# Performance work log

Measured on AMD Instinct MI355X. Metric: run time of the kernel, lower is better.

The kernel has to match this reference:

```python
import jax, jax.numpy as jnp
import numpy as np

HEADS = 8
CH = 256
DH = CH // HEADS  # 32
NB = 128          # nb_features
EPS = 1e-4


def setup_inputs() -> dict:
    key = jax.random.key(0)
    ks = jax.random.split(key, 8)
    b, c, h, w = 4, CH, 96, 96
    s = 1.0 / np.sqrt(CH)  # typical linear init scale
    x = jax.random.normal(ks[0], (b, c, h, w), dtype=jnp.float32)
    wq = jax.random.normal(ks[1], (CH, CH), dtype=jnp.float32) * s
    wk = jax.random.normal(ks[2], (CH, CH), dtype=jnp.float32) * s
    wv = jax.random.normal(ks[3], (CH, CH), dtype=jnp.float32) * s
    wo = jax.random.normal(ks[4], (CH, CH), dtype=jnp.float32) * s
    bo = jnp.zeros((CH,), dtype=jnp.float32)
    # FAVOR+ gaussian orthogonal random projection (nb_features, dim_head)
    pm = np.random.default_rng(0)
    blocks = []
    for _ in range(NB // DH):
        qmat, _ = np.linalg.qr(pm.standard_normal((DH, DH)))
        blocks.append(qmat.T)
    proj = np.concatenate(blocks, axis=0)
    # scale rows to chi-distributed norms (scaling=0 default in performer_pytorch)
    norms = np.linalg.norm(pm.standard_normal((NB, DH)), axis=1, keepdims=True)
    proj_mat = jnp.asarray(proj * norms, dtype=jnp.float32)
    wp = jax.random.normal(ks[5], (CH, CH, 1, 1), dtype=jnp.float32) * s
    bp = jnp.zeros((CH,), dtype=jnp.float32)
    return {"x": x, "wq": wq, "wk": wk, "wv": wv, "wo": wo, "bo": bo,
            "proj_mat": proj_mat, "wp": wp, "bp": bp}


def softmax_kernel(data, proj, is_query):
    # data: (b, h, n, d); proj: (m, d). Performer FAVOR+ positive softmax features.
    data_normalizer = data.shape[-1] ** -0.25
    ratio = proj.shape[0] ** -0.5
    data_dash = jnp.einsum('bhnd,md->bhnm', data * data_normalizer, proj)
    diag = (jnp.sum(data * data, axis=-1) * 0.5 * (data_normalizer ** 2))[..., None]
    if is_query:
        m = jnp.max(data_dash, axis=-1, keepdims=True)
    else:
        m = jnp.max(data_dash, axis=(-1, -2), keepdims=True)
    return ratio * (jnp.exp(data_dash - diag - m) + EPS)


def reference(x, wq, wk, wv, wo, bo, proj_mat, wp, bp):
    b, c, h, w = x.shape
    n = h * w
    xf = x.reshape(b, c, n).transpose(0, 2, 1)  # (b, n, c)

    def split_heads(t):
        return t.reshape(b, n, HEADS, DH).transpose(0, 2, 1, 3)  # (b, h, n, d)

    q = split_heads(xf @ wq.T)
    k = split_heads(xf @ wk.T)
    v = split_heads(xf @ wv.T)

    qp = softmax_kernel(q, proj_mat, True)   # (b, h, n, m)
    kp = softmax_kernel(k, proj_mat, False)  # (b, h, n, m)

    # non-causal linear attention
    k_sum = jnp.sum(kp, axis=-2)                                   # (b, h, m)
    d_inv = 1.0 / jnp.einsum('bhnm,bhm->bhn', qp, k_sum)           # (b, h, n)
    ctx = jnp.einsum('bhnm,bhnd->bhmd', kp, v)                     # (b, h, m, d)
    out = jnp.einsum('bhnm,bhmd->bhnd', qp, ctx) * d_inv[..., None]

    out = out.transpose(0, 2, 1, 3).reshape(b, n, c)  # merge heads
    out = out @ wo.T + bo                              # to_out (attn_out_bias=True)
    out = out.transpose(0, 2, 1).reshape(b, c, h, w)
    # 1x1 conv projection
    out = jnp.einsum('bchw,oc->bohw', out, wp[:, :, 0, 0]) + bp[None, :, None, None]
    return out
```

## Files before the change

### kernel.cpp

```cpp
#include <hip/hip_runtime.h>

#define NTOT 9216
#define NORMC 0.42044820762685725f
#define RATIO 0.08838834764831845f
#define FEPS 1e-4f

typedef _Float16 h8 __attribute__((ext_vector_type(8)));
typedef _Float16 h4 __attribute__((ext_vector_type(4)));
typedef float f4 __attribute__((ext_vector_type(4)));

__device__ __forceinline__ void gld16(const _Float16* g, _Float16* l) {
  __builtin_amdgcn_global_load_lds((const __attribute__((address_space(1))) void*)g,
                                   (__attribute__((address_space(3))) void*)l, 16, 0, 0);
}

__global__ __launch_bounds__(256) void prep(
    const float* __restrict__ x, const float* __restrict__ wq,
    const float* __restrict__ wk, const float* __restrict__ wv,
    const float* __restrict__ proj, const float* __restrict__ wo,
    const float* __restrict__ bo, const float* __restrict__ wp,
    const float* __restrict__ bp, _Float16* __restrict__ xT,
    _Float16* __restrict__ Wall, _Float16* __restrict__ projh,
    _Float16* __restrict__ Wc, float* __restrict__ bc) {
  __shared__ float T_s[64][65];
  int r = blockIdx.x, t = threadIdx.x;
  if (r < 2304) {
    int nx = r % 144, rem = r / 144;
    int cy = rem & 3, b = rem >> 2;
    int n0 = nx * 64, c0 = cy * 64;
    for (int i = 0; i < 4; ++i) {
      int f = t + i * 256;
      int cc = f >> 4, n4 = f & 15;
      float4 a = *(const float4*)(x + ((size_t)(b * 256 + c0 + cc)) * NTOT + n0 + n4 * 4);
      T_s[cc][n4 * 4 + 0] = a.x;
      T_s[cc][n4 * 4 + 1] = a.y;
      T_s[cc][n4 * 4 + 2] = a.z;
      T_s[cc][n4 * 4 + 3] = a.w;
    }
    __syncthreads();
    for (int i = 0; i < 2; ++i) {
      int f = t + i * 256;
      int nn = f >> 3, c8 = f & 7;
      h8 hv;
      for (int j = 0; j < 8; ++j) hv[j] = (_Float16)T_s[c8 * 8 + j][nn];
      *(h8*)(xT + ((size_t)(b * NTOT + n0 + nn)) * 256 + c0 + c8 * 8) = hv;
    }
    return;
  }
  int r2 = r - 2304;
  if (r2 < 768) {
    const float* src = (r2 < 256) ? wq + (size_t)r2 * 256
                     : (r2 < 512) ? wk + (size_t)(r2 - 256) * 256
                                  : wv + (size_t)(r2 - 512) * 256;
    Wall[(size_t)r2 * 256 + t] = (_Float16)src[t];
  } else if (r2 < 784) {
    int idx = (r2 - 768) * 256 + t;
    projh[idx] = (_Float16)proj[idx];
  } else {
    int o = r2 - 784;
    float acc = 0.f;
    for (int c = 0; c < 256; ++c) acc += wp[o * 256 + c] * wo[c * 256 + t];
    Wc[o * 256 + t] = (_Float16)acc;
    if (t == 0) {
      float ab = bp[o];
      for (int c = 0; c < 256; ++c) ab += wp[o * 256 + c] * bo[c];
      bc[o] = ab;
    }
  }
}

__global__ __launch_bounds__(256) void qkv_mfma(
    const _Float16* __restrict__ xT, const _Float16* __restrict__ Wall,
    const _Float16* __restrict__ projh, _Float16* __restrict__ q,
    _Float16* __restrict__ k, _Float16* __restrict__ vT,
    float* __restrict__ kmaxp) {
  __shared__ __align__(16) _Float16 pool[16384];
  int bx = blockIdx.x, co0 = blockIdx.y * 128, sel = blockIdx.z;
  int b = bx / 72, ntile = bx % 72;
  int n0 = bx * 128;
  const _Float16* Wb = Wall + (size_t)sel * 65536;
  int t = threadIdx.x, wave = t >> 6, lane = t & 63;
  int lm = lane & 15, lg = lane >> 4;
  int wm = (wave & 1) * 64, wn = (wave >> 1) * 64;
  int srow = wave * 32 + (lane >> 2);
  int scol = ((lane & 3) ^ ((lane >> 3) & 3)) * 8;
  const _Float16* gA = Wb + (size_t)(co0 + srow) * 256 + scol;
  const _Float16* gB = xT + (size_t)(n0 + srow) * 256 + scol;
  int so = wave * 1024;
  int pg = (lg ^ ((lm >> 1) & 3)) * 8;
  f4 acc[4][4] = {};
  gld16(gA, pool + so);
  gld16(gA + 16 * 256, pool + so + 512);
  gld16(gB, pool + 8192 + so);
  gld16(gB + 16 * 256, pool + 8192 + so + 512);
#pragma unroll 1
  for (int kt = 0; kt < 7; ++kt) {
    int cur = (kt & 1) << 12;
    int nxt = cur ^ 4096;
    int c0 = (kt + 1) * 32;
    gld16(gA + c0, pool + nxt + so);
    gld16(gA + c0 + 16 * 256, pool + nxt + so + 512);
    gld16(gB + c0, pool + 8192 + nxt + so);
    gld16(gB + c0 + 16 * 256, pool + 8192 + nxt + so + 512);
    asm volatile("s_waitcnt vmcnt(4)" ::: "memory");
    __builtin_amdgcn_s_barrier();
    __builtin_amdgcn_sched_barrier(0);
    h8 a[4], bf[4];
#pragma unroll
    for (int mi = 0; mi < 4; ++mi)
      a[mi] = *(const h8*)&pool[cur + (wm + mi * 16 + lm) * 32 + pg];
#pragma unroll
    for (int ni = 0; ni < 4; ++ni)
      bf[ni] = *(const h8*)&pool[8192 + cur + (wn + ni * 16 + lm) * 32 + pg];
    if (sel < 2) {
#pragma unroll
      for (int mi = 0; mi < 4; ++mi)
#pragma unroll
        for (int ni = 0; ni < 4; ++ni)
          acc[mi][ni] = __builtin_amdgcn_mfma_f32_16x16x32_f16(a[mi], bf[ni], acc[mi][ni], 0, 0, 0);
    } else {
#pragma unroll
      for (int mi = 0; mi < 4; ++mi)
#pragma unroll
        for (int ni = 0; ni < 4; ++ni)
          acc[mi][ni] = __builtin_amdgcn_mfma_f32_16x16x32_f16(bf[ni], a[mi], acc[mi][ni], 0, 0, 0);
    }
    __builtin_amdgcn_s_barrier();
  }
  {
    asm volatile("s_waitcnt vmcnt(0)" ::: "memory");
    __builtin_amdgcn_s_barrier();
    __builtin_amdgcn_sched_barrier(0);
    h8 a[4], bf[4];
#pragma unroll
    for (int mi = 0; mi < 4; ++mi)
      a[mi] = *(const h8*)&pool[4096 + (wm + mi * 16 + lm) * 32 + pg];
#pragma unroll
    for (int ni = 0; ni < 4; ++ni)
      bf[ni] = *(const h8*)&pool[8192 + 4096 + (wn + ni * 16 + lm) * 32 + pg];
    if (sel < 2) {
#pragma unroll
      for (int mi = 0; mi < 4; ++mi)
#pragma unroll
        for (int ni = 0; ni < 4; ++ni)
          acc[mi][ni] = __builtin_amdgcn_mfma_f32_16x16x32_f16(a[mi], bf[ni], acc[mi][ni], 0, 0, 0);
    } else {
#pragma unroll
      for (int mi = 0; mi < 4; ++mi)
#pragma unroll
        for (int ni = 0; ni < 4; ++ni)
          acc[mi][ni] = __builtin_amdgcn_mfma_f32_16x16x32_f16(bf[ni], a[mi], acc[mi][ni], 0, 0, 0);
    }
  }
  if (sel < 2) {
    _Float16* Out = (sel == 0) ? q : k;
#pragma unroll
    for (int mi = 0; mi < 4; ++mi)
#pragma unroll
      for (int ni = 0; ni < 4; ++ni) {
        h4 hv;
#pragma unroll
        for (int r = 0; r < 4; ++r) hv[r] = (_Float16)acc[mi][ni][r];
        *(h4*)(Out + (size_t)(n0 + wn + ni * 16 + lm) * 256 + co0 + wm + mi * 16 + lg * 4) = hv;
      }
    if (sel == 1) {
      _Float16* ktile = pool;
      h8 pr[8];
#pragma unroll
      for (int mt = 0; mt < 8; ++mt)
        pr[mt] = *(const h8*)&projh[(mt * 16 + lm) * 32 + lg * 8];
      float vmax = -1e30f;
      for (int half = 0; half < 2; ++half) {
        __syncthreads();
        if ((wave >> 1) == half) {
#pragma unroll
          for (int mi = 0; mi < 4; ++mi)
#pragma unroll
            for (int ni = 0; ni < 4; ++ni) {
              h4 hv;
#pragma unroll
              for (int r = 0; r < 4; ++r) hv[r] = (_Float16)acc[mi][ni][r];
              *(h4*)&ktile[(ni * 16 + lm) * 132 + wm + mi * 16 + lg * 4] = hv;
            }
        }
        __syncthreads();
#pragma unroll
        for (int nt2 = 0; nt2 < 4; ++nt2) {
          h8 a = *(const h8*)&ktile[(nt2 * 16 + lm) * 132 + wave * 32 + lg * 8];
#pragma unroll
          for (int mt = 0; mt < 8; ++mt) {
            f4 z = {0.f, 0.f, 0.f, 0.f};
            f4 d = __builtin_amdgcn_mfma_f32_16x16x32_f16(a, pr[mt], z, 0, 0, 0);
            vmax = fmaxf(vmax, fmaxf(fmaxf(d[0], d[1]), fmaxf(d[2], d[3])));
          }
        }
      }
      for (int i = 1; i < 64; i <<= 1) vmax = fmaxf(vmax, __shfl_xor(vmax, i, 64));
      if (lane == 0) {
        int h = (co0 >> 5) + wave;
        kmaxp[(size_t)(b * 8 + h) * 72 + ntile] = NORMC * vmax;
      }
    }
  } else {
#pragma unroll
    for (int mi = 0; mi < 4; ++mi)
#pragma unroll
      for (int ni = 0; ni < 4; ++ni) {
        h4 hv;
#pragma unroll
        for (int r = 0; r < 4; ++r) hv[r] = (_Float16)acc[mi][ni][r];
        *(h4*)(vT + ((size_t)(b * 256 + co0 + wm + mi * 16 + lm)) * NTOT +
               ntile * 128 + wn + ni * 16 + lg * 4) = hv;
      }
  }
}

__global__ __launch_bounds__(256) void ctx_mfma(
    const _Float16* __restrict__ k, const _Float16* __restrict__ vT,
    const _Float16* __restrict__ projh, const float* __restrict__ kmaxp,
    float* __restrict__ part) {
  __shared__ __align__(16) _Float16 k_s[128 * 32];
  __shared__ __align__(16) _Float16 vT_s[32 * 136];
  __shared__ __align__(16) _Float16 kpT[128 * 136];
  __shared__ float diag_s[128];
  __shared__ float kmax_sh;
  int bh = blockIdx.y, b = bh >> 3, h = bh & 7;
  int nbase = blockIdx.x * 384;
  int t = threadIdx.x, wave = t >> 6, lane = t & 63, lm = lane & 15, lg = lane >> 4;
  h8 pr[8];
#pragma unroll
  for (int mt = 0; mt < 8; ++mt) pr[mt] = *(const h8*)&projh[(mt * 16 + lm) * 32 + lg * 8];
  int scol = ((lane & 3) ^ ((lane >> 3) & 3)) * 8;
  const _Float16* gK =
      k + ((size_t)(b * NTOT + nbase + wave * 32 + (lane >> 2))) * 256 + h * 32 + scol;
  const _Float16* gV = vT + ((size_t)(b * 256 + h * 32 + (t >> 3))) * NTOT + nbase;
  _Float16* lK = k_s + wave * 1024;
  int vd = t >> 3, vg = t & 7;
  gld16(gK, lK);
  gld16(gK + 16 * 256, lK + 512);
  h8 vr0 = *(const h8*)(gV + vg * 8);
  h8 vr1 = *(const h8*)(gV + 64 + vg * 8);
  {
    float* kred = (float*)kpT;
    if (t < 72) kred[t] = kmaxp[(size_t)bh * 72 + t];
    __syncthreads();
    if (t == 0) {
      float mx = -1e30f;
      for (int i = 0; i < 72; ++i) mx = fmaxf(mx, kred[i]);
      kmax_sh = mx;
    }
    __syncthreads();
  }
  float kmax = kmax_sh;
  int pg = (lg ^ ((lm >> 1) & 3)) * 8;
  f4 cacc[2][2] = {};
  float ks[8] = {};
#pragma unroll 1
  for (int ch = 0; ch < 3; ++ch) {
    *(h8*)&vT_s[vd * 136 + vg * 8] = vr0;
    *(h8*)&vT_s[vd * 136 + 64 + vg * 8] = vr1;
    asm volatile("s_waitcnt vmcnt(0) lgkmcnt(0)" ::: "memory");
    __builtin_amdgcn_s_barrier();
    __builtin_amdgcn_sched_barrier(0);
    if (t < 128) {
      float s = 0.f;
#pragma unroll
      for (int c = 0; c < 4; ++c) {
        h8 kv = *(const h8*)&k_s[t * 32 + c * 8];
#pragma unroll
        for (int j = 0; j < 8; ++j) s += (float)kv[j] * (float)kv[j];
      }
      diag_s[t] = s * (0.5f * NORMC * NORMC);
    }
    f4 dsh[2][8];
#pragma unroll
    for (int nt = 0; nt < 2; ++nt) {
      h8 a = *(const h8*)&k_s[(wave * 32 + nt * 16 + lm) * 32 + pg];
#pragma unroll
      for (int mt = 0; mt < 8; ++mt) {
        f4 z = {0.f, 0.f, 0.f, 0.f};
        dsh[nt][mt] = __builtin_amdgcn_mfma_f32_16x16x32_f16(a, pr[mt], z, 0, 0, 0);
      }
    }
    asm volatile("s_waitcnt lgkmcnt(0)" ::: "memory");
    __builtin_amdgcn_s_barrier();
    __builtin_amdgcn_sched_barrier(0);
    if (ch < 2) {
      gld16(gK + (size_t)((ch + 1) * 128) * 256, lK);
      gld16(gK + (size_t)((ch + 1) * 128) * 256 + 16 * 256, lK + 512);
      vr0 = *(const h8*)(gV + (ch + 1) * 128 + vg * 8);
      vr1 = *(const h8*)(gV + (ch + 1) * 128 + 64 + vg * 8);
    }
#pragma unroll
    for (int nt = 0; nt < 2; ++nt)
#pragma unroll
      for (int mt = 0; mt < 8; ++mt) {
        h4 hv;
        float lsum = 0.f;
#pragma unroll
        for (int r = 0; r < 4; ++r) {
          int nl = wave * 32 + nt * 16 + lg * 4 + r;
          float val = RATIO * (__expf(NORMC * dsh[nt][mt][r] - diag_s[nl] - kmax) + FEPS);
          hv[r] = (_Float16)val;
          lsum += val;
        }
        ks[mt] += lsum;
        *(h4*)&kpT[(mt * 16 + lm) * 136 + wave * 32 + nt * 16 + lg * 4] = hv;
      }
    asm volatile("s_waitcnt lgkmcnt(0)" ::: "memory");
    __builtin_amdgcn_s_barrier();
    __builtin_amdgcn_sched_barrier(0);
#pragma unroll
    for (int k2 = 0; k2 < 4; ++k2) {
      h8 a2[2], b2[2];
#pragma unroll
      for (int mt2 = 0; mt2 < 2; ++mt2)
        a2[mt2] = *(const h8*)&kpT[(wave * 32 + mt2 * 16 + lm) * 136 + k2 * 32 + lg * 8];
#pragma unroll
      for (int dt = 0; dt < 2; ++dt)
        b2[dt] = *(const h8*)&vT_s[(dt * 16 + lm) * 136 + k2 * 32 + lg * 8];
#pragma unroll
      for (int mt2 = 0; mt2 < 2; ++mt2)
#pragma unroll
        for (int dt = 0; dt < 2; ++dt)
          cacc[mt2][dt] =
              __builtin_amdgcn_mfma_f32_16x16x32_f16(a2[mt2], b2[dt], cacc[mt2][dt], 0, 0, 0);
    }
    __builtin_amdgcn_s_barrier();
  }
  float* pp = part + (size_t)(blockIdx.y * 24 + blockIdx.x) * 4224;
#pragma unroll
  for (int mt2 = 0; mt2 < 2; ++mt2)
#pragma unroll
    for (int dt = 0; dt < 2; ++dt)
      *(f4*)(pp + (dt * 16 + lm) * 128 + wave * 32 + mt2 * 16 + lg * 4) = cacc[mt2][dt];
  float* redk = (float*)kpT;
#pragma unroll
  for (int mt = 0; mt < 8; ++mt) {
    float s = ks[mt];
    s += __shfl_xor(s, 16, 64);
    s += __shfl_xor(s, 32, 64);
    if (lg == 0) redk[wave * 128 + mt * 16 + lm] = s;
  }
  __syncthreads();
  if (t < 128)
    pp[32 * 128 + t] = redk[t] + redk[128 + t] + redk[256 + t] + redk[384 + t];
}

__global__ __launch_bounds__(256) void reduce_ctx(
    const float* __restrict__ part, _Float16* __restrict__ ctxT_g,
    float* __restrict__ ksum_g) {
  int bh = blockIdx.x >> 2, qtr = blockIdx.x & 3;
  int t = threadIdx.x;
  const float* pb = part + (size_t)bh * 24 * 4224;
  for (int it = 0; it < 5; ++it) {
    int lc = it * 256 + t;
    if (lc < 1056) {
      int cell = qtr * 1056 + lc;
      float s = 0.f;
      for (int p = 0; p < 24; ++p) s += pb[(size_t)p * 4224 + cell];
      int d = cell >> 7, m = cell & 127;
      if (d < 32) ctxT_g[(size_t)bh * 4096 + d * 128 + m] = (_Float16)s;
      else ksum_g[(size_t)bh * 128 + m] = s;
    }
  }
}

__global__ __launch_bounds__(256) void attn_mfma(
    const _Float16* __restrict__ q, const _Float16* __restrict__ projh,
    const _Float16* __restrict__ ctxT_g, const float* __restrict__ ksum_g,
    _Float16* __restrict__ attn) {
  __shared__ __align__(16) _Float16 q_sh[128 * 32];
  __shared__ __align__(16) _Float16 qp_s[128 * 136];
  __shared__ float ksum_s[128];
  int n0 = blockIdx.x * 128;
  int bh = blockIdx.y, b = bh >> 3, h = bh & 7;
  int t = threadIdx.x, wave = t >> 6, lane = t & 63, lm = lane & 15, lg = lane >> 4;
  h8 pr[8];
#pragma unroll
  for (int mt = 0; mt < 8; ++mt) pr[mt] = *(const h8*)&projh[(mt * 16 + lm) * 32 + lg * 8];
  int scol = ((lane & 3) ^ ((lane >> 3) & 3)) * 8;
  const _Float16* gQ =
      q + ((size_t)(b * NTOT + n0 + wave * 32 + (lane >> 2))) * 256 + h * 32 + scol;
  gld16(gQ, q_sh + wave * 1024);
  gld16(gQ + 16 * 256, q_sh + wave * 1024 + 512);
  h8 ac[2][4];
#pragma unroll
  for (int dt = 0; dt < 2; ++dt)
#pragma unroll
    for (int k2 = 0; k2 < 4; ++k2)
      ac[dt][k2] = *(const h8*)&ctxT_g[(size_t)bh * 4096 + (dt * 16 + lm) * 128 + k2 * 32 + lg * 8];
  if (t < 128) ksum_s[t] = ksum_g[(size_t)bh * 128 + t];
  __syncthreads();
  int pg = (lg ^ ((lm >> 1) & 3)) * 8;
  float diag_r[2];
#pragma unroll
  for (int nt = 0; nt < 2; ++nt) {
    int n = wave * 32 + nt * 16 + lm;
    float s = 0.f;
#pragma unroll
    for (int c = 0; c < 4; ++c) {
      h8 qv = *(const h8*)&q_sh[n * 32 + c * 8];
#pragma unroll
      for (int j = 0; j < 8; ++j) s += (float)qv[j] * (float)qv[j];
    }
    diag_r[nt] = s * (0.5f * NORMC * NORMC);
  }
  f4 dsh[2][8];
#pragma unroll
  for (int nt = 0; nt < 2; ++nt) {
    h8 qf = *(const h8*)&q_sh[(wave * 32 + nt * 16 + lm) * 32 + pg];
#pragma unroll
    for (int mt = 0; mt < 8; ++mt) {
      f4 z = {0.f, 0.f, 0.f, 0.f};
      dsh[nt][mt] = __builtin_amdgcn_mfma_f32_16x16x32_f16(pr[mt], qf, z, 0, 0, 0);
    }
  }
  float den_r[2];
#pragma unroll
  for (int nt = 0; nt < 2; ++nt) {
    float mx = -1e30f;
#pragma unroll
    for (int mt = 0; mt < 8; ++mt)
#pragma unroll
      for (int r = 0; r < 4; ++r) mx = fmaxf(mx, dsh[nt][mt][r]);
    mx = fmaxf(mx, __shfl_xor(mx, 16, 64));
    mx = fmaxf(mx, __shfl_xor(mx, 32, 64));
    float den = 0.f;
#pragma unroll
    for (int mt = 0; mt < 8; ++mt) {
      h4 hv;
#pragma unroll
      for (int r = 0; r < 4; ++r) {
        float val = RATIO * (__expf(NORMC * (dsh[nt][mt][r] - mx) - diag_r[nt]) + FEPS);
        hv[r] = (_Float16)val;
        den += val * ksum_s[mt * 16 + lg * 4 + r];
      }
      *(h4*)&qp_s[(wave * 32 + nt * 16 + lm) * 136 + mt * 16 + lg * 4] = hv;
    }
    den += __shfl_xor(den, 16, 64);
    den += __shfl_xor(den, 32, 64);
    den_r[nt] = 1.f / den;
  }
  __syncthreads();
  f4 oacc[2][2] = {};
#pragma unroll
  for (int k2 = 0; k2 < 4; ++k2) {
    h8 bq[2];
#pragma unroll
    for (int nt = 0; nt < 2; ++nt)
      bq[nt] = *(const h8*)&qp_s[(wave * 32 + nt * 16 + lm) * 136 + k2 * 32 + lg * 8];
#pragma unroll
    for (int dt = 0; dt < 2; ++dt)
#pragma unroll
      for (int nt = 0; nt < 2; ++nt)
        oacc[dt][nt] = __builtin_amdgcn_mfma_f32_16x16x32_f16(ac[dt][k2], bq[nt], oacc[dt][nt], 0, 0, 0);
  }
#pragma unroll
  for (int dt = 0; dt < 2; ++dt)
#pragma unroll
    for (int nt = 0; nt < 2; ++nt) {
      int n = wave * 32 + nt * 16 + lm;
      h4 hv;
#pragma unroll
      for (int r = 0; r < 4; ++r) hv[r] = (_Float16)(oacc[dt][nt][r] * den_r[nt]);
      *(h4*)(attn + ((size_t)(b * NTOT + n0 + n)) * 256 + h * 32 + dt * 16 + lg * 4) = hv;
    }
}

__global__ __launch_bounds__(256) void out_mfma(
    const _Float16* __restrict__ Wc, const _Float16* __restrict__ attn,
    const float* __restrict__ bc, float* __restrict__ out) {
  __shared__ __align__(16) _Float16 pool[16384];
  int bx = blockIdx.x;
  int o0 = blockIdx.y * 128;
  int b = bx / 72, nb0 = (bx % 72) * 128;
  int t = threadIdx.x, wave = t >> 6, lane = t & 63;
  int lm = lane & 15, lg = lane >> 4;
  int wm = (wave & 1) * 64, wn = (wave >> 1) * 64;
  int srow = wave * 32 + (lane >> 2);
  int scol = ((lane & 3) ^ ((lane >> 3) & 3)) * 8;
  const _Float16* gA = Wc + (size_t)(o0 + srow) * 256 + scol;
  const _Float16* gB = attn + (size_t)(b * NTOT + nb0 + srow) * 256 + scol;
  int so = wave * 1024;
  int pg = (lg ^ ((lm >> 1) & 3)) * 8;
  f4 acc[4][4] = {};
  gld16(gA, pool + so);
  gld16(gA + 16 * 256, pool + so + 512);
  gld16(gB, pool + 8192 + so);
  gld16(gB + 16 * 256, pool + 8192 + so + 512);
#pragma unroll 1
  for (int kt = 0; kt < 7; ++kt) {
    int cur = (kt & 1) << 12;
    int nxt = cur ^ 4096;
    int c0 = (kt + 1) * 32;
    gld16(gA + c0, pool + nxt + so);
    gld16(gA + c0 + 16 * 256, pool + nxt + so + 512);
    gld16(gB + c0, pool + 8192 + nxt + so);
    gld16(gB + c0 + 16 * 256, pool + 8192 + nxt + so + 512);
    asm volatile("s_waitcnt vmcnt(4)" ::: "memory");
    __builtin_amdgcn_s_barrier();
    __builtin_amdgcn_sched_barrier(0);
    h8 a[4], bf[4];
#pragma unroll
    for (int mi = 0; mi < 4; ++mi)
      a[mi] = *(const h8*)&pool[cur + (wm + mi * 16 + lm) * 32 + pg];
#pragma unroll
    for (int ni = 0; ni < 4; ++ni)
      bf[ni] = *(const h8*)&pool[8192 + cur + (wn + ni * 16 + lm) * 32 + pg];
#pragma unroll
    for (int mi = 0; mi < 4; ++mi)
#pragma unroll
      for (int ni = 0; ni < 4; ++ni)
        acc[mi][ni] = __builtin_amdgcn_mfma_f32_16x16x32_f16(bf[ni], a[mi], acc[mi][ni], 0, 0, 0);
    __builtin_amdgcn_s_barrier();
  }
  {
    asm volatile("s_waitcnt vmcnt(0)" ::: "memory");
    __builtin_amdgcn_s_barrier();
    __builtin_amdgcn_sched_barrier(0);
    h8 a[4], bf[4];
#pragma unroll
    for (int mi = 0; mi < 4; ++mi)
      a[mi] = *(const h8*)&pool[4096 + (wm + mi * 16 + lm) * 32 + pg];
#pragma unroll
    for (int ni = 0; ni < 4; ++ni)
      bf[ni] = *(const h8*)&pool[8192 + 4096 + (wn + ni * 16 + lm) * 32 + pg];
#pragma unroll
    for (int mi = 0; mi < 4; ++mi)
#pragma unroll
      for (int ni = 0; ni < 4; ++ni)
        acc[mi][ni] = __builtin_amdgcn_mfma_f32_16x16x32_f16(bf[ni], a[mi], acc[mi][ni], 0, 0, 0);
  }
#pragma unroll
  for (int mi = 0; mi < 4; ++mi) {
    int o = o0 + wm + mi * 16 + lm;
    float bias = bc[o];
#pragma unroll
    for (int ni = 0; ni < 4; ++ni) {
      f4 ov = acc[mi][ni];
      float4 st = make_float4(ov[0] + bias, ov[1] + bias, ov[2] + bias, ov[3] + bias);
      *(float4*)(out + ((size_t)(b * 256 + o)) * NTOT + nb0 + wn + ni * 16 + lg * 4) = st;
    }
  }
}

extern "C" void kernel_launch(void* const* d_in, const int* in_sizes, int n_in,
                              void* d_out, int out_size, void* d_ws, size_t ws_size,
                              hipStream_t stream) {
  const float* x = (const float*)d_in[0];
  const float* wq = (const float*)d_in[1];
  const float* wk = (const float*)d_in[2];
  const float* wv = (const float*)d_in[3];
  const float* wo = (const float*)d_in[4];
  const float* bo = (const float*)d_in[5];
  const float* proj = (const float*)d_in[6];
  const float* wp = (const float*)d_in[7];
  const float* bp = (const float*)d_in[8];
  float* out = (float*)d_out;
  float* ws = (float*)d_ws;

  float* part = ws;
  float* kmaxp = part + 3244032;
  float* ksum_g = kmaxp + 2304;
  float* bc = ksum_g + 4096;
  _Float16* hb = (_Float16*)(bc + 256);
  const size_t THALF = (size_t)4 * NTOT * 256;
  _Float16* q_h = hb;
  _Float16* k_h = q_h + THALF;
  _Float16* xT = k_h + THALF;
  _Float16* vTg = xT + THALF;
  _Float16* Wall = vTg + THALF;
  _Float16* Wc = Wall + 768 * 256;
  _Float16* projh = Wc + 65536;
  _Float16* ctxT_g = projh + 4096;

  prep<<<3344, 256, 0, stream>>>(x, wq, wk, wv, proj, wo, bo, wp, bp,
                                 xT, Wall, projh, Wc, bc);
  qkv_mfma<<<dim3(288, 2, 3), 256, 0, stream>>>(xT, Wall, projh, q_h, k_h, vTg, kmaxp);
  ctx_mfma<<<dim3(24, 32), 256, 0, stream>>>(k_h, vTg, projh, kmaxp, part);
  reduce_ctx<<<128, 256, 0, stream>>>(part, ctxT_g, ksum_g);
  attn_mfma<<<dim3(72, 32), 256, 0, stream>>>(q_h, projh, ctxT_g, ksum_g, xT);
  out_mfma<<<dim3(288, 2), 256, 0, stream>>>(Wc, xT, bc, out);
}
```

Measured before the change: 217.1 us.

## Fuse Q, K, V projections into one block sharing the activation tile

The QKV GEMM kernel now computes all three projections in a single block, loading each activation tile once into shared memory and reusing it against the Wq, Wk and Wv tiles. The grid drops its third dimension. This removes the repeated global loads of xT across three separate blocks and folds the tail iteration into the main loop. In exchange, each block holds three accumulator sets (48 f4 registers) and double-buffers 64KB of LDS, which can lower occupancy and raise register pressure. The out GEMM loop gets the same tail folding.

```diff
diff --git a/kernel.cpp b/kernel.cpp
--- a/kernel.cpp
+++ b/kernel.cpp
@@ -74,144 +74,125 @@
     const _Float16* __restrict__ projh, _Float16* __restrict__ q,
     _Float16* __restrict__ k, _Float16* __restrict__ vT,
     float* __restrict__ kmaxp) {
-  __shared__ __align__(16) _Float16 pool[16384];
-  int bx = blockIdx.x, co0 = blockIdx.y * 128, sel = blockIdx.z;
+  __shared__ __align__(16) _Float16 pool[32768];
+  int bx = blockIdx.x, co0 = blockIdx.y * 128;
   int b = bx / 72, ntile = bx % 72;
   int n0 = bx * 128;
-  const _Float16* Wb = Wall + (size_t)sel * 65536;
   int t = threadIdx.x, wave = t >> 6, lane = t & 63;
   int lm = lane & 15, lg = lane >> 4;
   int wm = (wave & 1) * 64, wn = (wave >> 1) * 64;
   int srow = wave * 32 + (lane >> 2);
   int scol = ((lane & 3) ^ ((lane >> 3) & 3)) * 8;
-  const _Float16* gA = Wb + (size_t)(co0 + srow) * 256 + scol;
   const _Float16* gB = xT + (size_t)(n0 + srow) * 256 + scol;
+  const _Float16* gWq = Wall + (size_t)(co0 + srow) * 256 + scol;
+  const _Float16* gWk = gWq + 65536;
+  const _Float16* gWv = gWq + 131072;
   int so = wave * 1024;
   int pg = (lg ^ ((lm >> 1) & 3)) * 8;
-  f4 acc[4][4] = {};
-  gld16(gA, pool + so);
-  gld16(gA + 16 * 256, pool + so + 512);
-  gld16(gB, pool + 8192 + so);
-  gld16(gB + 16 * 256, pool + 8192 + so + 512);
+  f4 acc_q[4][4] = {}, acc_k[4][4] = {}, acc_v[4][4] = {};
+  gld16(gB, pool + so);
+  gld16(gB + 16 * 256, pool + so + 512);
+  gld16(gWq, pool + 4096 + so);
+  gld16(gWq + 16 * 256, pool + 4096 + so + 512);
+  gld16(gWk, pool + 8192 + so);
+  gld16(gWk + 16 * 256, pool + 8192 + so + 512);
+  gld16(gWv, pool + 12288 + so);
+  gld16(gWv + 16 * 256, pool + 12288 + so + 512);
 #pragma unroll 1
-  for (int kt = 0; kt < 7; ++kt) {
-    int cur = (kt & 1) << 12;
-    int nxt = cur ^ 4096;
-    int c0 = (kt + 1) * 32;
-    gld16(gA + c0, pool + nxt + so);
-    gld16(gA + c0 + 16 * 256, pool + nxt + so + 512);
-    gld16(gB + c0, pool + 8192 + nxt + so);
-    gld16(gB + c0 + 16 * 256, pool + 8192 + nxt + so + 512);
-    asm volatile("s_waitcnt vmcnt(4)" ::: "memory");
+  for (int kt = 0; kt < 8; ++kt) {
+    int cur = (kt & 1) << 14;
+    int nxt = cur ^ 16384;
+    if (kt < 7) {
+      int c0 = (kt + 1) * 32;
+      gld16(gB + c0, pool + nxt + so);
+      gld16(gB + c0 + 16 * 256, pool + nxt + so + 512);
+      gld16(gWq + c0, pool + nxt + 4096 + so);
+      gld16(gWq + c0 + 16 * 256, pool + nxt + 4096 + so + 512);
+      gld16(gWk + c0, pool + nxt + 8192 + so);
+      gld16(gWk + c0 + 16 * 256, pool + nxt + 8192 + so + 512);
+      gld16(gWv + c0, pool + nxt + 12288 + so);
+      gld16(gWv + c0 + 16 * 256, pool + nxt + 12288 + so + 512);
+      asm volatile("s_waitcnt vmcnt(8)" ::: "memory");
+    } else {
+      asm volatile("s_waitcnt vmcnt(0)" ::: "memory");
+    }
     __builtin_amdgcn_s_barrier();
     __builtin_amdgcn_sched_barrier(0);
-    h8 a[4], bf[4];
+    h8 bf[4], aq[4], ak[4], av[4];
+#pragma unroll
+    for (int ni = 0; ni < 4; ++ni)
+      bf[ni] = *(const h8*)&pool[cur + (wn + ni * 16 + lm) * 32 + pg];
+#pragma unroll
+    for (int mi = 0; mi < 4; ++mi) {
+      int ro = (wm + mi * 16 + lm) * 32 + pg;
+      aq[mi] = *(const h8*)&pool[cur + 4096 + ro];
+      ak[mi] = *(const h8*)&pool[cur + 8192 + ro];
+      av[mi] = *(const h8*)&pool[cur + 12288 + ro];
+    }
 #pragma unroll
     for (int mi = 0; mi < 4; ++mi)
-      a[mi] = *(const h8*)&pool[cur + (wm + mi * 16 + lm) * 32 + pg];
-#pragma unroll
-    for (int ni = 0; ni < 4; ++ni)
-      bf[ni] = *(const h8*)&pool[8192 + cur + (wn + ni * 16 + lm) * 32 + pg];
-    if (sel < 2) {
-#pragma unroll
-      for (int mi = 0; mi < 4; ++mi)
-#pragma unroll
-        for (int ni = 0; ni < 4; ++ni)
-          acc[mi][ni] = __builtin_amdgcn_mfma_f32_16x16x32_f16(a[mi], bf[ni], acc[mi][ni], 0, 0, 0);
-    } else {
-#pragma unroll
-      for (int mi = 0; mi < 4; ++mi)
-#pragma unroll
-        for (int ni = 0; ni < 4; ++ni)
-          acc[mi][ni] = __builtin_amdgcn_mfma_f32_16x16x32_f16(bf[ni], a[mi], acc[mi][ni], 0, 0, 0);
-    }
-    __builtin_amdgcn_s_barrier();
-  }
+#pragma unroll
+      for (int ni = 0; ni < 4; ++ni) {
+        acc_q[mi][ni] = __builtin_amdgcn_mfma_f32_16x16x32_f16(aq[mi], bf[ni], acc_q[mi][ni], 0, 0, 0);
+        acc_k[mi][ni] = __builtin_amdgcn_mfma_f32_16x16x32_f16(ak[mi], bf[ni], acc_k[mi][ni], 0, 0, 0);
+        acc_v[mi][ni] = __builtin_amdgcn_mfma_f32_16x16x32_f16(bf[ni], av[mi], acc_v[mi][ni], 0, 0, 0);
+      }
+    __builtin_amdgcn_s_barrier();
+  }
+#pragma unroll
+  for (int mi = 0; mi < 4; ++mi)
+#pragma unroll
+    for (int ni = 0; ni < 4; ++ni) {
+      h4 hq, hk, hv;
+#pragma unroll
+      for (int r = 0; r < 4; ++r) {
+        hq[r] = (_Float16)acc_q[mi][ni][r];
+        hk[r] = (_Float16)acc_k[mi][ni][r];
+        hv[r] = (_Float16)acc_v[mi][ni][r];
+      }
+      size_t nidx = (size_t)(n0 + wn + ni * 16 + lm) * 256 + co0 + wm + mi * 16 + lg * 4;
+      *(h4*)(q + nidx) = hq;
+      *(h4*)(k + nidx) = hk;
+      *(h4*)(vT + ((size_t)(b * 256 + co0 + wm + mi * 16 + lm)) * NTOT +
+             ntile * 128 + wn + ni * 16 + lg * 4) = hv;
+    }
   {
-    asm volatile("s_waitcnt vmcnt(0)" ::: "memory");
-    __builtin_amdgcn_s_barrier();
-    __builtin_amdgcn_sched_barrier(0);
-    h8 a[4], bf[4];
-#pragma unroll
-    for (int mi = 0; mi < 4; ++mi)
-      a[mi] = *(const h8*)&pool[4096 + (wm + mi * 16 + lm) * 32 + pg];
-#pragma unroll
-    for (int ni = 0; ni < 4; ++ni)
-      bf[ni] = *(const h8*)&pool[8192 + 4096 + (wn + ni * 16 + lm) * 32 + pg];
-    if (sel < 2) {
-#pragma unroll
-      for (int mi = 0; mi < 4; ++mi)
-#pragma unroll
-        for (int ni = 0; ni < 4; ++ni)
-          acc[mi][ni] = __builtin_amdgcn_mfma_f32_16x16x32_f16(a[mi], bf[ni], acc[mi][ni], 0, 0, 0);
-    } else {
-#pragma unroll
-      for (int mi = 0; mi < 4; ++mi)
-#pragma unroll
-        for (int ni = 0; ni < 4; ++ni)
-          acc[mi][ni] = __builtin_amdgcn_mfma_f32_16x16x32_f16(bf[ni], a[mi], acc[mi][ni], 0, 0, 0);
-    }
-  }
-  if (sel < 2) {
-    _Float16* Out = (sel == 0) ? q : k;
-#pragma unroll
-    for (int mi = 0; mi < 4; ++mi)
-#pragma unroll
-      for (int ni = 0; ni < 4; ++ni) {
-        h4 hv;
-#pragma unroll
-        for (int r = 0; r < 4; ++r) hv[r] = (_Float16)acc[mi][ni][r];
-        *(h4*)(Out + (size_t)(n0 + wn + ni * 16 + lm) * 256 + co0 + wm + mi * 16 + lg * 4) = hv;
-      }
-    if (sel == 1) {
-      _Float16* ktile = pool;
-      h8 pr[8];
-#pragma unroll
-      for (int mt = 0; mt < 8; ++mt)
-        pr[mt] = *(const h8*)&projh[(mt * 16 + lm) * 32 + lg * 8];
-      float vmax = -1e30f;
-      for (int half = 0; half < 2; ++half) {
-        __syncthreads();
-        if ((wave >> 1) == half) {
-#pragma unroll
-          for (int mi = 0; mi < 4; ++mi)
-#pragma unroll
-            for (int ni = 0; ni < 4; ++ni) {
-              h4 hv;
-#pragma unroll
-              for (int r = 0; r < 4; ++r) hv[r] = (_Float16)acc[mi][ni][r];
-              *(h4*)&ktile[(ni * 16 + lm) * 132 + wm + mi * 16 + lg * 4] = hv;
-            }
+    _Float16* ktile = pool;
+    h8 pr[8];
+#pragma unroll
+    for (int mt = 0; mt < 8; ++mt)
+      pr[mt] = *(const h8*)&projh[(mt * 16 + lm) * 32 + lg * 8];
+    float vmax = -1e30f;
+    for (int half = 0; half < 2; ++half) {
+      __syncthreads();
+      if ((wave >> 1) == half) {
+#pragma unroll
+        for (int mi = 0; mi < 4; ++mi)
+#pragma unroll
+          for (int ni = 0; ni < 4; ++ni) {
+            h4 hv;
+#pragma unroll
+            for (int r = 0; r < 4; ++r) hv[r] = (_Float16)acc_k[mi][ni][r];
+            *(h4*)&ktile[(ni * 16 + lm) * 132 + wm + mi * 16 + lg * 4] = hv;
+          }
+      }
+      __syncthreads();
+#pragma unroll
+      for (int nt2 = 0; nt2 < 4; ++nt2) {
+        h8 a = *(const h8*)&ktile[(nt2 * 16 + lm) * 132 + wave * 32 + lg * 8];
+#pragma unroll
+        for (int mt = 0; mt < 8; ++mt) {
+          f4 z = {0.f, 0.f, 0.f, 0.f};
+          f4 d = __builtin_amdgcn_mfma_f32_16x16x32_f16(a, pr[mt], z, 0, 0, 0);
+          vmax = fmaxf(vmax, fmaxf(fmaxf(d[0], d[1]), fmaxf(d[2], d[3])));
         }
-        __syncthreads();
-#pragma unroll
-        for (int nt2 = 0; nt2 < 4; ++nt2) {
-          h8 a = *(const h8*)&ktile[(nt2 * 16 + lm) * 132 + wave * 32 + lg * 8];
-#pragma unroll
-          for (int mt = 0; mt < 8; ++mt) {
-            f4 z = {0.f, 0.f, 0.f, 0.f};
-            f4 d = __builtin_amdgcn_mfma_f32_16x16x32_f16(a, pr[mt], z, 0, 0, 0);
-            vmax = fmaxf(vmax, fmaxf(fmaxf(d[0], d[1]), fmaxf(d[2], d[3])));
-          }
-        }
-      }
-      for (int i = 1; i < 64; i <<= 1) vmax = fmaxf(vmax, __shfl_xor(vmax, i, 64));
-      if (lane == 0) {
-        int h = (co0 >> 5) + wave;
-        kmaxp[(size_t)(b * 8 + h) * 72 + ntile] = NORMC * vmax;
-      }
-    }
-  } else {
-#pragma unroll
-    for (int mi = 0; mi < 4; ++mi)
-#pragma unroll
-      for (int ni = 0; ni < 4; ++ni) {
-        h4 hv;
-#pragma unroll
-        for (int r = 0; r < 4; ++r) hv[r] = (_Float16)acc[mi][ni][r];
-        *(h4*)(vT + ((size_t)(b * 256 + co0 + wm + mi * 16 + lm)) * NTOT +
-               ntile * 128 + wn + ni * 16 + lg * 4) = hv;
-      }
+      }
+    }
+    for (int i = 1; i < 64; i <<= 1) vmax = fmaxf(vmax, __shfl_xor(vmax, i, 64));
+    if (lane == 0) {
+      int h = (co0 >> 5) + wave;
+      kmaxp[(size_t)(b * 8 + h) * 72 + ntile] = NORMC * vmax;
+    }
   }
 }
 
@@ -490,15 +471,19 @@
   gld16(gB, pool + 8192 + so);
   gld16(gB + 16 * 256, pool + 8192 + so + 512);
 #pragma unroll 1
-  for (int kt = 0; kt < 7; ++kt) {
+  for (int kt = 0; kt < 8; ++kt) {
     int cur = (kt & 1) << 12;
     int nxt = cur ^ 4096;
-    int c0 = (kt + 1) * 32;
-    gld16(gA + c0, pool + nxt + so);
-    gld16(gA + c0 + 16 * 256, pool + nxt + so + 512);
-    gld16(gB + c0, pool + 8192 + nxt + so);
-    gld16(gB + c0 + 16 * 256, pool + 8192 + nxt + so + 512);
-    asm volatile("s_waitcnt vmcnt(4)" ::: "memory");
+    if (kt < 7) {
+      int c0 = (kt + 1) * 32;
+      gld16(gA + c0, pool + nxt + so);
+      gld16(gA + c0 + 16 * 256, pool + nxt + so + 512);
+      gld16(gB + c0, pool + 8192 + nxt + so);
+      gld16(gB + c0 + 16 * 256, pool + 8192 + nxt + so + 512);
+      asm volatile("s_waitcnt vmcnt(4)" ::: "memory");
+    } else {
+      asm volatile("s_waitcnt vmcnt(0)" ::: "memory");
+    }
     __builtin_amdgcn_s_barrier();
     __builtin_amdgcn_sched_barrier(0);
     h8 a[4], bf[4];
@@ -514,23 +499,6 @@
       for (int ni = 0; ni < 4; ++ni)
         acc[mi][ni] = __builtin_amdgcn_mfma_f32_16x16x32_f16(bf[ni], a[mi], acc[mi][ni], 0, 0, 0);
     __builtin_amdgcn_s_barrier();
-  }
-  {
-    asm volatile("s_waitcnt vmcnt(0)" ::: "memory");
-    __builtin_amdgcn_s_barrier();
-    __builtin_amdgcn_sched_barrier(0);
-    h8 a[4], bf[4];
-#pragma unroll
-    for (int mi = 0; mi < 4; ++mi)
-      a[mi] = *(const h8*)&pool[4096 + (wm + mi * 16 + lm) * 32 + pg];
-#pragma unroll
-    for (int ni = 0; ni < 4; ++ni)
-      bf[ni] = *(const h8*)&pool[8192 + 4096 + (wn + ni * 16 + lm) * 32 + pg];
-#pragma unroll
-    for (int mi = 0; mi < 4; ++mi)
-#pragma unroll
-      for (int ni = 0; ni < 4; ++ni)
-        acc[mi][ni] = __builtin_amdgcn_mfma_f32_16x16x32_f16(bf[ni], a[mi], acc[mi][ni], 0, 0, 0);
   }
 #pragma unroll
   for (int mi = 0; mi < 4; ++mi) {
@@ -577,7 +545,7 @@
 
   prep<<<3344, 256, 0, stream>>>(x, wq, wk, wv, proj, wo, bo, wp, bp,
                                  xT, Wall, projh, Wc, bc);
-  qkv_mfma<<<dim3(288, 2, 3), 256, 0, stream>>>(xT, Wall, projh, q_h, k_h, vTg, kmaxp);
+  qkv_mfma<<<dim3(288, 2), 256, 0, stream>>>(xT, Wall, projh, q_h, k_h, vTg, kmaxp);
   ctx_mfma<<<dim3(24, 32), 256, 0, stream>>>(k_h, vTg, projh, kmaxp, part);
   reduce_ctx<<<128, 256, 0, stream>>>(part, ctxT_g, ksum_g);
   attn_mfma<<<dim3(72, 32), 256, 0, stream>>>(q_h, projh, ctxT_g, ksum_g, xT);
```

Result: slower. 232.9 us (+7.3%).
